# Kernel optimization log

Hardware: AMD Instinct MI355X
Metric: run time of the kernel (lower is better)

Reference implementation:

```python
import math
import jax, jax.numpy as jnp
import numpy as np

HID = 2048
H = 16
HKV = 8
D = HID // H          # 128 head_dim
F = D                 # feature_dim = head_dim
SEQ = 2048
BATCH = 2
THETA = 10000.0


def setup_inputs() -> dict:
    key = jax.random.key(0)
    ks = jax.random.split(key, 10)
    s = lambda k, shape, scale=0.02: (jax.random.normal(k, shape, dtype=jnp.float32) * scale)
    return {
        "hidden_states": jax.random.normal(ks[0], (BATCH, SEQ, HID), dtype=jnp.float32),
        "Wq": s(ks[1], (HID, HID)),
        "bq": s(ks[2], (HID,)),
        "Wk": s(ks[3], (HKV * D, HID)),
        "bk": s(ks[4], (HKV * D,)),
        "Wv": s(ks[5], (HKV * D, HID)),
        "bv": s(ks[6], (HKV * D,)),
        "Wo": s(ks[7], (HID, HID)),
        "bo": s(ks[8], (HID,)),
        "rand_matrix": jax.random.normal(ks[9], (F // 2, D), dtype=jnp.float32),
    }


def _rotate_half(x):
    x1, x2 = x[..., : x.shape[-1] // 2], x[..., x.shape[-1] // 2 :]
    return jnp.concatenate((-x2, x1), axis=-1)


def _softmax_kernel(x, R):
    # L2-normalize last dim (norm clamped at 1e-6), project, [sin, cos] features
    n = jnp.sqrt(jnp.sum(x * x, axis=-1, keepdims=True))
    x = x / jnp.maximum(n, 1e-6)
    p = jnp.einsum("...d,ed->...e", x, R)          # [..., F/2]
    feats = jnp.concatenate([jnp.sin(p), jnp.cos(p)], axis=-1)
    return feats / math.sqrt(F)


def reference(hidden_states, Wq, bq, Wk, bk, Wv, bv, Wo, bo, rand_matrix):
    b, s, _ = hidden_states.shape
    q = (hidden_states @ Wq.T + bq).reshape(b, s, H, D).transpose(0, 2, 1, 3)    # bhsd
    k = (hidden_states @ Wk.T + bk).reshape(b, s, HKV, D).transpose(0, 2, 1, 3)
    v = (hidden_states @ Wv.T + bv).reshape(b, s, HKV, D).transpose(0, 2, 1, 3)

    # RoPE (default position_ids = arange)
    inv_freq = 1.0 / (THETA ** (jnp.arange(0, D, 2, dtype=jnp.float32) / D))     # [D/2]
    freqs = jnp.arange(s, dtype=jnp.float32)[:, None] * inv_freq[None, :]        # [s, D/2]
    emb = jnp.concatenate((freqs, freqs), axis=-1)                               # [s, D]
    cos = jnp.cos(emb)[None, None, :, :]
    sin = jnp.sin(emb)[None, None, :, :]
    q = q * cos + _rotate_half(q) * sin
    k = k * cos + _rotate_half(k) * sin

    # GQA repeat (repeat_interleave along head axis)
    rep = H // HKV
    k = jnp.repeat(k, rep, axis=1)
    v = jnp.repeat(v, rep, axis=1)

    qp = _softmax_kernel(q, rand_matrix)   # [b,H,s,F]
    kp = _softmax_kernel(k, rand_matrix)   # [b,H,s,F]

    # Faithful to source einsums: contraction over the HEAD axis
    # torch: 'bsnd,bsnh->bndh' with tensors laid out (b, head, seq, dim)
    kv = jnp.einsum("bhsf,bhsd->bsfd", kp, v)        # [b, s, F, D]
    out = jnp.einsum("bhsf,bsfd->bhsd", qp, kv)      # [b, H, s, D]
    out = out.reshape(b, s, HID)                      # flat reshape, as in source
    return out @ Wo.T + bo
```

## Files before the change

kernel.cpp:

```cpp
#include <hip/hip_runtime.h>
#include <stdint.h>

typedef unsigned short ushort_t;
typedef __bf16 bf16x8 __attribute__((ext_vector_type(8)));
typedef float f32x4 __attribute__((ext_vector_type(4)));
typedef unsigned int u32;

__device__ __forceinline__ float bf2f(ushort_t u) {
    union { u32 u; float f; } x; x.u = ((u32)u) << 16; return x.f;
}
__device__ __forceinline__ ushort_t f2bf(float f) {
    union { float f; u32 u; } x; x.f = f;
    u32 r = x.u + 0x7FFFu + ((x.u >> 16) & 1u);
    return (ushort_t)(r >> 16);
}

__device__ __forceinline__ void async16(const void* gp, void* lp) {
    __builtin_amdgcn_global_load_lds(
        (const __attribute__((address_space(1))) u32*)(gp),
        (__attribute__((address_space(3))) u32*)(lp),
        16, 0, 0);
}

template<int N>
__device__ __forceinline__ void wait_barrier() {
    asm volatile("s_waitcnt vmcnt(%0)\n\ts_barrier" :: "n"(N) : "memory");
}

__global__ __launch_bounds__(256) void cast_all_kernel(
    const float* __restrict__ hs, const float* __restrict__ Wq,
    const float* __restrict__ Wk, const float* __restrict__ Wv,
    const float* __restrict__ Wo, const float* __restrict__ Rm,
    const float* __restrict__ bq, const float* __restrict__ bk,
    const float* __restrict__ bv,
    ushort_t* __restrict__ Xb, ushort_t* __restrict__ Wcat,
    ushort_t* __restrict__ Wo16, ushort_t* __restrict__ Rbf,
    float* __restrict__ bcat)
{
    int bid = blockIdx.x;
    if (bid == 10244) {
        for (int i = threadIdx.x; i < 4096; i += 256) {
            float v = (i < 2048) ? bq[i] : (i < 3072) ? bk[i - 2048] : bv[i - 3072];
            bcat[i] = v;
        }
        return;
    }
    const float* src; ushort_t* dst; int base;
    if (bid < 4096)       { src = hs; dst = Xb;              base = bid; }
    else if (bid < 6144)  { src = Wq; dst = Wcat;            base = bid - 4096; }
    else if (bid < 7168)  { src = Wk; dst = Wcat + 4194304;  base = bid - 6144; }
    else if (bid < 8192)  { src = Wv; dst = Wcat + 6291456;  base = bid - 7168; }
    else if (bid < 10240) { src = Wo; dst = Wo16;            base = bid - 8192; }
    else                  { src = Rm; dst = Rbf;             base = bid - 10240; }
    int i = base * 2048 + threadIdx.x * 8;
    float4 v0 = *reinterpret_cast<const float4*>(src + i);
    float4 v1 = *reinterpret_cast<const float4*>(src + i + 4);
    ushort_t o[8];
    o[0] = f2bf(v0.x); o[1] = f2bf(v0.y); o[2] = f2bf(v0.z); o[3] = f2bf(v0.w);
    o[4] = f2bf(v1.x); o[5] = f2bf(v1.y); o[6] = f2bf(v1.z); o[7] = f2bf(v1.w);
    *reinterpret_cast<uint4*>(dst + i) = *reinterpret_cast<const uint4*>(o);
}

#define CLOSE_PLAIN __builtin_amdgcn_s_barrier()
#define CLOSE_VM(nn) do { asm volatile("s_waitcnt vmcnt(%0)" :: "n"(nn) : "memory"); \
                          __builtin_amdgcn_s_barrier(); } while (0)
#define SBAR __builtin_amdgcn_sched_barrier(0)

template<int BM, int MBLK, int NBLK, int KC, bool STORE_BF16>
__global__ __launch_bounds__(512, 2) void gemm8r_kernel(
    const ushort_t* __restrict__ A, const ushort_t* __restrict__ B,
    const float* __restrict__ bias, void* __restrict__ C,
    const int M, const int N)
{
    constexpr int NT  = KC / 64;
    constexpr int NI  = NT / 2;
    constexpr int MF2 = BM / 64;
    constexpr int NFR = BM / 32;
    constexpr int AH  = BM * 64;
    constexpr int SH  = BM / 128;
    constexpr int BUF = 2 * AH + 32768;
    constexpr int TI  = 2 * SH + 4;
    static_assert(NT % 2 == 0 && NI >= 3, "need even NT >= 6");
    __shared__ alignas(16) char lds[2 * BUF];

    const int tid  = threadIdx.x;
    const int wid  = tid >> 6;
    const int lane = tid & 63;
    const int wm = wid >> 2, wn = wid & 3;

    constexpr int XN  = NBLK / 8;
    constexpr int NXR = 8 / XN;
    constexpr int RH  = MBLK / NXR;
    const int x  = blockIdx.x & 7;
    const int kb = blockIdx.x >> 3;
    const int mb = (x % NXR) * RH + (kb >> 3);
    const int nb = (x / NXR) * 8 + (kb & 7);
    const int am0 = mb * BM, bn0 = nb * 256;

    const int sr3 = tid >> 3;
    const int c8  = tid & 7;
    const int cs  = c8 ^ (sr3 & 7);
    const long K2 = (long)KC * 2;
    const char* agp = (const char*)A + (size_t)(am0 + sr3) * K2 + cs * 16;
    const char* bgp = (const char*)B + (size_t)(bn0 + sr3) * K2 + cs * 16;
    const int ldsw = wid << 10;

    const int fr = lane & 15, fc = lane >> 4;
    const int sw0 = ((fc)     ^ (fr & 7)) * 16;
    const int sw1 = ((4 + fc) ^ (fr & 7)) * 16;
    const int abase = wm * AH + fr * 128;
    const int bbase = 2 * AH + wn * 8192 + fr * 128;

    f32x4 acc[NFR][4] = {};
    bf16x8 afX[MF2], afY[MF2], bfX[4], bfY[4];

    auto stage_half = [&](const char* gp, int rowoff, int bufb, int off,
                          long kof, int niss) {
        char* lp = lds + bufb + off + ldsw;
        const char* g = gp + (size_t)rowoff * K2 + kof;
#pragma unroll
        for (int i = 0; i < niss; ++i)
            async16(g + (size_t)(i * 64) * K2, lp + i * 8192);
    };
#define SA0(T) stage_half(agp, 0,      ((T) & 1) * BUF, 0,          (long)(T) * 128, SH)
#define SA1(T) stage_half(agp, BM / 2, ((T) & 1) * BUF, AH,         (long)(T) * 128, SH)
#define SB0(T) stage_half(bgp, 0,      ((T) & 1) * BUF, 2 * AH,     (long)(T) * 128, 2)
#define SB1(T) stage_half(bgp, 128,    ((T) & 1) * BUF, 2 * AH + 16384, (long)(T) * 128, 2)

    auto rdA = [&](bf16x8 (&dst)[MF2], int bufb, int h, int kc) {
        const char* lp_ = lds + bufb;
        const int sw_ = kc ? sw1 : sw0;
#pragma unroll
        for (int j = 0; j < MF2; ++j)
            dst[j] = *(const bf16x8*)(lp_ + abase + (h * MF2 + j) * 2048 + sw_);
    };
    auto rdB = [&](bf16x8 (&dst)[4], int bufb, int kc) {
        const char* lp_ = lds + bufb;
        const int sw_ = kc ? sw1 : sw0;
#pragma unroll
        for (int n = 0; n < 4; ++n)
            dst[n] = *(const bf16x8*)(lp_ + bbase + n * 2048 + sw_);
    };
    auto domf = [&](bf16x8 (&af)[MF2], bf16x8 (&bf)[4], int h) {
        __builtin_amdgcn_s_setprio(1);
#pragma unroll
        for (int j = 0; j < MF2; ++j)
#pragma unroll
            for (int n = 0; n < 4; ++n)
                acc[h * MF2 + j][n] = __builtin_amdgcn_mfma_f32_16x16x32_bf16(
                    af[j], bf[n], acc[h * MF2 + j][n], 0, 0, 0);
        __builtin_amdgcn_s_setprio(0);
    };

#define QT(b, S0, C0, S1, C1, S2, C2, S3, C3) do {                 \
    rdA(afX, b, 0, 0); rdB(bfX, b, 0); rdA(afY, b, 1, 0);          \
    S0; SBAR; domf(afX, bfX, 0); C0;                               \
    rdA(afX, b, 0, 1); rdB(bfY, b, 1);                             \
    S1; SBAR; domf(afY, bfX, 1); C1;                               \
    rdA(afY, b, 1, 1);                                             \
    S2; SBAR; domf(afX, bfY, 0); C2;                               \
    S3; SBAR; domf(afY, bfY, 1); C3;                               \
} while (0)

    SA0(0); SA1(0); SB0(0); SB1(0);
    SA0(1); SA1(1); SB0(1); SB1(1);
    wait_barrier<TI>();

    QT(0,   (void)0, CLOSE_PLAIN, (void)0, CLOSE_PLAIN,
            (void)0, CLOSE_PLAIN, SB0(2),  CLOSE_VM(2));
    QT(BUF, SB1(2),  CLOSE_PLAIN, SA0(2),  CLOSE_PLAIN,
            SA1(2),  CLOSE_PLAIN, SB0(3),  CLOSE_VM(2));

    for (int i = 1; i <= NI - 2; ++i) {
        const int t = 2 * i;
        QT(0,   SB1(t + 1), CLOSE_PLAIN, SA0(t + 1), CLOSE_PLAIN,
                SA1(t + 1), CLOSE_PLAIN, SB0(t + 2), CLOSE_VM(2));
        QT(BUF, SB1(t + 2), CLOSE_PLAIN, SA0(t + 2), CLOSE_PLAIN,
                SA1(t + 2), CLOSE_PLAIN, SB0(t + 3), CLOSE_VM(2));
    }

    {
        constexpr int T1 = NT - 1;
        QT(0,   SB1(T1), CLOSE_PLAIN, SA0(T1), CLOSE_PLAIN,
                SA1(T1), CLOSE_PLAIN, (void)0, CLOSE_VM(0));
        QT(BUF, (void)0, CLOSE_PLAIN, (void)0, CLOSE_PLAIN,
                (void)0, CLOSE_PLAIN, (void)0, CLOSE_PLAIN);
    }

    const int crow0 = fc << 2;
#pragma unroll
    for (int m = 0; m < NFR; ++m) {
        const int row_b = am0 + wm * (BM / 2) + m * 16 + crow0;
#pragma unroll
        for (int n = 0; n < 4; ++n) {
            const int col = bn0 + wn * 64 + n * 16 + fr;
            const float bs = bias[col];
#pragma unroll
            for (int r = 0; r < 4; ++r) {
                const float v = acc[m][n][r] + bs;
                if (STORE_BF16)
                    ((ushort_t*)C)[(size_t)(row_b + r) * N + col] = f2bf(v);
                else
                    ((float*)C)[(size_t)(row_b + r) * N + col] = v;
            }
        }
    }
#undef QT
#undef SA0
#undef SA1
#undef SB0
#undef SB1
}

__global__ __launch_bounds__(256) void fused_attn_kernel(
    const ushort_t* __restrict__ qkv, const ushort_t* __restrict__ Rbf,
    ushort_t* __restrict__ ctx)
{
    __shared__ ushort_t xnb[32][136];
    __shared__ ushort_t fpb[32][136];
    __shared__ float vsm[8][132];
    __shared__ float Am[16][20];

    const int tok = blockIdx.x;
    const int b = tok >> 11, s = tok & 2047;
    const int tid = threadIdx.x;
    const int wid = tid >> 6, lane = tid & 63;
    const ushort_t* row = qkv + (size_t)tok * 4096;

    float invf = exp2f(-(float)lane * (13.287712379549449f / 64.0f));
    float ang = (float)s * invf;
    float sn, cs;
    __sincosf(ang, &sn, &cs);
#pragma unroll
    for (int i = 0; i < 6; ++i) {
        int vec = wid * 6 + i;
        int base = (vec < 16) ? vec * 128 : 2048 + (vec - 16) * 128;
        float a = bf2f(row[base + lane]);
        float c = bf2f(row[base + lane + 64]);
        float ra = a * cs - c * sn;
        float rc = c * cs + a * sn;
        float ss2 = ra * ra + rc * rc;
#pragma unroll
        for (int off = 32; off; off >>= 1) ss2 += __shfl_xor(ss2, off);
        float inv = 1.0f / fmaxf(sqrtf(ss2), 1e-6f);
        xnb[vec][lane]      = f2bf(ra * inv);
        xnb[vec][lane + 64] = f2bf(rc * inv);
    }
    for (int idx = tid; idx < 1024; idx += 256)
        vsm[idx >> 7][idx & 127] = bf2f(row[3072 + idx]);
    __syncthreads();

    {
        const int fr = lane & 15, fc = lane >> 4;
        f32x4 pacc[2] = {};
#pragma unroll
        for (int kc = 0; kc < 4; ++kc) {
            bf16x8 bfrag = *reinterpret_cast<const bf16x8*>(
                Rbf + (wid * 16 + fr) * 128 + kc * 32 + fc * 8);
            bf16x8 a0 = *reinterpret_cast<const bf16x8*>(&xnb[fr][kc * 32 + fc * 8]);
            bf16x8 a1 = *reinterpret_cast<const bf16x8*>(&xnb[16 + fr][kc * 32 + fc * 8]);
            pacc[0] = __builtin_amdgcn_mfma_f32_16x16x32_bf16(a0, bfrag, pacc[0], 0, 0, 0);
            pacc[1] = __builtin_amdgcn_mfma_f32_16x16x32_bf16(a1, bfrag, pacc[1], 0, 0, 0);
        }
        const int e = wid * 16 + fr;
#pragma unroll
        for (int m = 0; m < 2; ++m) {
            if (m == 1 && fc >= 2) break;
#pragma unroll
            for (int r = 0; r < 4; ++r) {
                int vec = m * 16 + fc * 4 + r;
                float sp, cp;
                __sincosf(pacc[m][r], &sp, &cp);
                fpb[vec][e]      = f2bf(sp * 0.08838834764831845f);
                fpb[vec][e + 64] = f2bf(cp * 0.08838834764831845f);
            }
        }
    }
    __syncthreads();

    if (wid == 0) {
        const int fr = lane & 15, fc = lane >> 4;
        f32x4 aacc = {};
#pragma unroll
        for (int kc = 0; kc < 4; ++kc) {
            bf16x8 qa = *reinterpret_cast<const bf16x8*>(&fpb[fr][kc * 32 + fc * 8]);
            bf16x8 ka = *reinterpret_cast<const bf16x8*>(&fpb[16 + fr][kc * 32 + fc * 8]);
            aacc = __builtin_amdgcn_mfma_f32_16x16x32_bf16(qa, ka, aacc, 0, 0, 0);
        }
        if (fr < 8)
#pragma unroll
            for (int r = 0; r < 4; ++r)
                Am[fc * 4 + r][fr] = 2.0f * aacc[r];
    }
    __syncthreads();

    for (int g = tid; g < 512; g += 256) {
        int h = g >> 5;
        int d0 = (g & 31) << 2;
        float4 a = make_float4(0.f, 0.f, 0.f, 0.f);
#pragma unroll
        for (int hk = 0; hk < 8; ++hk) {
            float am = Am[h][hk];
            float4 v = *reinterpret_cast<const float4*>(&vsm[hk][d0]);
            a.x = fmaf(am, v.x, a.x); a.y = fmaf(am, v.y, a.y);
            a.z = fmaf(am, v.z, a.z); a.w = fmaf(am, v.w, a.w);
        }
        int orow = (b << 11) + (h << 7) + (s >> 4);
        int ocol = ((s & 15) << 7) + d0;
        ushort4 o;
        o.x = f2bf(a.x); o.y = f2bf(a.y); o.z = f2bf(a.z); o.w = f2bf(a.w);
        *reinterpret_cast<ushort4*>(&ctx[(size_t)orow * 2048 + ocol]) = o;
    }
}

extern "C" void kernel_launch(void* const* d_in, const int* in_sizes, int n_in,
                              void* d_out, int out_size, void* d_ws, size_t ws_size,
                              hipStream_t stream)
{
    const float* hs = (const float*)d_in[0];
    const float* Wq = (const float*)d_in[1];
    const float* bq = (const float*)d_in[2];
    const float* Wk = (const float*)d_in[3];
    const float* bk = (const float*)d_in[4];
    const float* Wv = (const float*)d_in[5];
    const float* bv = (const float*)d_in[6];
    const float* Wo = (const float*)d_in[7];
    const float* bo = (const float*)d_in[8];
    const float* Rm = (const float*)d_in[9];
    float* out = (float*)d_out;

    char* ws = (char*)d_ws;
    ushort_t* Xb   = (ushort_t*)(ws);
    ushort_t* Wcat = (ushort_t*)(ws + 16777216);
    ushort_t* Wo16 = (ushort_t*)(ws + 33554432);
    ushort_t* qkv  = (ushort_t*)(ws + 41943040);
    ushort_t* ctx  = (ushort_t*)(ws + 75497472);
    float*    bcat = (float*)   (ws + 92274688);
    ushort_t* Rbf  = (ushort_t*)(ws + 92291072);

    cast_all_kernel<<<10245, 256, 0, stream>>>(hs, Wq, Wk, Wv, Wo, Rm,
                                               bq, bk, bv,
                                               Xb, Wcat, Wo16, Rbf, bcat);

    gemm8r_kernel<256, 16, 16, 2048, true><<<256, 512, 0, stream>>>(
        Xb, Wcat, bcat, qkv, 4096, 4096);

    fused_attn_kernel<<<4096, 256, 0, stream>>>(qkv, Rbf, ctx);

    gemm8r_kernel<128, 32, 8, 2048, false><<<256, 512, 0, stream>>>(
        ctx, Wo16, bo, out, 4096, 2048);
}
```

Before: 140.8 us.

## Add phased double-buffered GEMM variant with interleaved staging for output projection

Adds a new GEMM kernel that splits each K-tile into four phases, issuing async global-to-LDS loads for the next tile between MFMA phases, with barriers and raised wave priority around the MFMA blocks. It is used only for the output projection GEMM. The goal is better overlap of memory loads with matrix-core work and fewer stalls per K step, at the cost of more barriers and added code complexity. It also declares two blocks per CU via launch bounds.

```diff
diff --git a/kernel.cpp b/kernel.cpp
--- a/kernel.cpp
+++ b/kernel.cpp
@@ -212,6 +212,151 @@
 #undef SB1
 }
 
+template<int BM, int MBLK, int NBLK, int KC, bool STORE_BF16>
+__global__ __launch_bounds__(512, 2) void gemm8p_kernel(
+    const ushort_t* __restrict__ A, const ushort_t* __restrict__ B,
+    const float* __restrict__ bias, void* __restrict__ C,
+    const int M, const int N)
+{
+    constexpr int NT  = KC / 64;
+    constexpr int NI  = NT / 2;
+    constexpr int MF2 = BM / 64;
+    constexpr int NFR = BM / 32;
+    constexpr int AH  = BM * 64;
+    constexpr int SH  = BM / 128;
+    constexpr int BUF = 2 * AH + 32768;
+    constexpr int TI  = 2 * SH + 4;
+    static_assert(NT % 2 == 0 && NI >= 3, "need even NT >= 6");
+    __shared__ alignas(16) char lds[2 * BUF];
+
+    const int tid  = threadIdx.x;
+    const int wid  = tid >> 6;
+    const int lane = tid & 63;
+    const int wm = wid >> 2, wn = wid & 3;
+
+    constexpr int XN  = NBLK / 8;
+    constexpr int NXR = 8 / XN;
+    constexpr int RH  = MBLK / NXR;
+    const int x  = blockIdx.x & 7;
+    const int kb = blockIdx.x >> 3;
+    const int mb = (x % NXR) * RH + (kb >> 3);
+    const int nb = (x / NXR) * 8 + (kb & 7);
+    const int am0 = mb * BM, bn0 = nb * 256;
+
+    const int sr3 = tid >> 3;
+    const int c8  = tid & 7;
+    const int cs  = c8 ^ (sr3 & 7);
+    const long K2 = (long)KC * 2;
+    const char* agp = (const char*)A + (size_t)(am0 + sr3) * K2 + cs * 16;
+    const char* bgp = (const char*)B + (size_t)(bn0 + sr3) * K2 + cs * 16;
+    const int ldsw = wid << 10;
+
+    const int fr = lane & 15, fc = lane >> 4;
+    const int sw0 = ((fc)     ^ (fr & 7)) * 16;
+    const int sw1 = ((4 + fc) ^ (fr & 7)) * 16;
+    const int abase = wm * AH + fr * 128;
+    const int bbase = 2 * AH + wn * 8192 + fr * 128;
+
+    f32x4 acc[NFR][4] = {};
+    bf16x8 bf[4];
+
+    auto stage_half = [&](const char* gp, int rowoff, int bufb, int off,
+                          long kof, int niss) {
+        char* lp = lds + bufb + off + ldsw;
+        const char* g = gp + (size_t)rowoff * K2 + kof;
+#pragma unroll
+        for (int i = 0; i < niss; ++i)
+            async16(g + (size_t)(i * 64) * K2, lp + i * 8192);
+    };
+#define SA0(T) stage_half(agp, 0,      ((T) & 1) * BUF, 0,          (long)(T) * 128, SH)
+#define SA1(T) stage_half(agp, BM / 2, ((T) & 1) * BUF, AH,         (long)(T) * 128, SH)
+#define SB0(T) stage_half(bgp, 0,      ((T) & 1) * BUF, 2 * AH,     (long)(T) * 128, 2)
+#define SB1(T) stage_half(bgp, 128,    ((T) & 1) * BUF, 2 * AH + 16384, (long)(T) * 128, 2)
+
+#define PH(h, kc, bufb, STG, CLOSE) do {                                      \
+    const char* lp_ = lds + (bufb);                                           \
+    const int sw_ = (kc) ? sw1 : sw0;                                         \
+    if ((h) == 0) {                                                           \
+        _Pragma("unroll") for (int n = 0; n < 4; ++n)                         \
+            bf[n] = *(const bf16x8*)(lp_ + bbase + n * 2048 + sw_);           \
+    }                                                                         \
+    bf16x8 af_[MF2];                                                          \
+    _Pragma("unroll") for (int j = 0; j < MF2; ++j)                           \
+        af_[j] = *(const bf16x8*)(lp_ + abase + ((h) * MF2 + j) * 2048 + sw_);\
+    STG;                                                                      \
+    __builtin_amdgcn_s_barrier();                                             \
+    asm volatile("s_waitcnt lgkmcnt(0)" ::: "memory");                        \
+    __builtin_amdgcn_s_setprio(1);                                            \
+    _Pragma("unroll") for (int j = 0; j < MF2; ++j)                           \
+    _Pragma("unroll") for (int n = 0; n < 4; ++n)                             \
+        acc[(h) * MF2 + j][n] = __builtin_amdgcn_mfma_f32_16x16x32_bf16(      \
+            af_[j], bf[n], acc[(h) * MF2 + j][n], 0, 0, 0);                   \
+    __builtin_amdgcn_s_setprio(0);                                            \
+    CLOSE;                                                                    \
+} while (0)
+
+    SA0(0); SA1(0); SB0(0); SB1(0);
+    SA0(1); SA1(1); SB0(1); SB1(1);
+    wait_barrier<TI>();
+
+    PH(0, 0, 0,    (void)0,  CLOSE_PLAIN);
+    PH(1, 0, 0,    (void)0,  CLOSE_PLAIN);
+    PH(0, 1, 0,    (void)0,  CLOSE_PLAIN);
+    PH(1, 1, 0,    SB0(2),   CLOSE_VM(2));
+    PH(0, 0, BUF,  SB1(2),   CLOSE_PLAIN);
+    PH(1, 0, BUF,  SA0(2),   CLOSE_PLAIN);
+    PH(0, 1, BUF,  SA1(2),   CLOSE_PLAIN);
+    PH(1, 1, BUF,  SB0(3),   CLOSE_VM(2));
+
+    for (int i = 1; i <= NI - 2; ++i) {
+        const int t = 2 * i;
+        PH(0, 0, 0,    SB1(t + 1), CLOSE_PLAIN);
+        PH(1, 0, 0,    SA0(t + 1), CLOSE_PLAIN);
+        PH(0, 1, 0,    SA1(t + 1), CLOSE_PLAIN);
+        PH(1, 1, 0,    SB0(t + 2), CLOSE_VM(2));
+        PH(0, 0, BUF,  SB1(t + 2), CLOSE_PLAIN);
+        PH(1, 0, BUF,  SA0(t + 2), CLOSE_PLAIN);
+        PH(0, 1, BUF,  SA1(t + 2), CLOSE_PLAIN);
+        PH(1, 1, BUF,  SB0(t + 3), CLOSE_VM(2));
+    }
+
+    {
+        constexpr int T1 = NT - 1;
+        PH(0, 0, 0,    SB1(T1),  CLOSE_PLAIN);
+        PH(1, 0, 0,    SA0(T1),  CLOSE_PLAIN);
+        PH(0, 1, 0,    SA1(T1),  CLOSE_PLAIN);
+        PH(1, 1, 0,    (void)0,  CLOSE_VM(0));
+        PH(0, 0, BUF,  (void)0,  CLOSE_PLAIN);
+        PH(1, 0, BUF,  (void)0,  CLOSE_PLAIN);
+        PH(0, 1, BUF,  (void)0,  CLOSE_PLAIN);
+        PH(1, 1, BUF,  (void)0,  CLOSE_PLAIN);
+    }
+
+    const int crow0 = fc << 2;
+#pragma unroll
+    for (int m = 0; m < NFR; ++m) {
+        const int row_b = am0 + wm * (BM / 2) + m * 16 + crow0;
+#pragma unroll
+        for (int n = 0; n < 4; ++n) {
+            const int col = bn0 + wn * 64 + n * 16 + fr;
+            const float bs = bias[col];
+#pragma unroll
+            for (int r = 0; r < 4; ++r) {
+                const float v = acc[m][n][r] + bs;
+                if (STORE_BF16)
+                    ((ushort_t*)C)[(size_t)(row_b + r) * N + col] = f2bf(v);
+                else
+                    ((float*)C)[(size_t)(row_b + r) * N + col] = v;
+            }
+        }
+    }
+#undef PH
+#undef SA0
+#undef SA1
+#undef SB0
+#undef SB1
+}
+
 __global__ __launch_bounds__(256) void fused_attn_kernel(
     const ushort_t* __restrict__ qkv, const ushort_t* __restrict__ Rbf,
     ushort_t* __restrict__ ctx)
@@ -347,6 +492,6 @@
 
     fused_attn_kernel<<<4096, 256, 0, stream>>>(qkv, Rbf, ctx);
 
-    gemm8r_kernel<128, 32, 8, 2048, false><<<256, 512, 0, stream>>>(
+    gemm8p_kernel<128, 32, 8, 2048, false><<<256, 512, 0, stream>>>(
         ctx, Wo16, bo, out, 4096, 2048);
 }
```

Result: no change. 139.7 us (median of 2 runs) (-0.8%).
